# Kernel tuning notes

Measured on AMD Instinct MI355X. Metric: run time of the kernel, lower is better.

The kernel has to match this reference:

```python
import jax, jax.numpy as jnp
import numpy as np

N, E, G = 50000, 800000, 64
IN, HID, HEADS, OUT = 128, 64, 4, 128
NEG = 0.2  # PyG GATConv default negative_slope


def setup_inputs() -> dict:
    key = jax.random.key(0)
    ks = jax.random.split(key, 12)
    nrm = lambda k, shape, s: (jax.random.normal(k, shape, jnp.float32) * s)
    x = nrm(ks[0], (N, IN), 1.0)
    edge_index = jax.random.randint(ks[1], (2, E), 0, N)
    batch = jnp.sort(jax.random.randint(ks[2], (N,), 0, G))
    W1 = nrm(ks[3], (IN, HEADS * HID), IN ** -0.5)
    a1_src = nrm(ks[4], (HEADS, HID), HID ** -0.5)
    a1_dst = nrm(ks[5], (HEADS, HID), HID ** -0.5)
    b1 = jnp.zeros((HEADS * HID,), jnp.float32)
    W2 = nrm(ks[6], (HEADS * HID, OUT), (HEADS * HID) ** -0.5)
    a2_src = nrm(ks[7], (1, OUT), OUT ** -0.5)
    a2_dst = nrm(ks[8], (1, OUT), OUT ** -0.5)
    b2 = jnp.zeros((OUT,), jnp.float32)
    fc_W = nrm(ks[9], (OUT, OUT), OUT ** -0.5)
    fc_b = jnp.zeros((OUT,), jnp.float32)
    return dict(x=x, edge_index=edge_index, batch=batch, W1=W1, a1_src=a1_src,
                a1_dst=a1_dst, b1=b1, W2=W2, a2_src=a2_src, a2_dst=a2_dst,
                b2=b2, fc_W=fc_W, fc_b=fc_b)


def gat_conv(x, W, a_src, a_dst, b, src, dst, heads):
    n = x.shape[0]
    ch = W.shape[1] // heads
    h = (x @ W).reshape(n, heads, ch)                      # [n, H, C]
    al_s = jnp.einsum('nhc,hc->nh', h, a_src)              # per-node src logits
    al_d = jnp.einsum('nhc,hc->nh', h, a_dst)
    e = al_s[src] + al_d[dst]                              # [E, H]
    e = jnp.where(e > 0, e, NEG * e)                       # LeakyReLU
    # segment softmax over incoming edges of each dst node
    m = jax.lax.stop_gradient(jax.ops.segment_max(e, dst, num_segments=n))
    m = jnp.where(jnp.isfinite(m), m, 0.0)
    ex = jnp.exp(e - m[dst])
    s = jax.ops.segment_sum(ex, dst, num_segments=n)
    alpha = ex / (s[dst] + 1e-16)                          # [E, H]
    out = jax.ops.segment_sum(h[src] * alpha[..., None], dst, num_segments=n)
    return out.reshape(n, heads * ch) + b                  # concat heads + bias


def reference(x, edge_index, batch, W1, a1_src, a1_dst, b1, W2, a2_src, a2_dst, b2, fc_W, fc_b):
    loops = jnp.arange(N, dtype=edge_index.dtype)          # PyG adds self-loops
    src = jnp.concatenate([edge_index[0], loops])
    dst = jnp.concatenate([edge_index[1], loops])
    h = jax.nn.elu(gat_conv(x, W1, a1_src, a1_dst, b1, src, dst, HEADS))
    h = jax.nn.elu(gat_conv(h, W2, a2_src, a2_dst, b2, src, dst, 1))
    sums = jax.ops.segment_sum(h, batch, num_segments=G)
    cnt = jax.ops.segment_sum(jnp.ones((N,), h.dtype), batch, num_segments=G)
    pooled = sums / jnp.maximum(cnt, 1.0)[:, None]         # global mean pool
    return jax.nn.relu(pooled @ fc_W + fc_b)
```

## Files before the change

kernel.cpp:

```cpp
#include <hip/hip_runtime.h>
#include <math.h>

#define N_NODES 50000
#define N_EDGES 800000
#define N_GRAPHS 64
#define NEG 0.2f

typedef unsigned short us;
typedef us us2 __attribute__((ext_vector_type(2)));
typedef us us4 __attribute__((ext_vector_type(4)));
typedef us us8 __attribute__((ext_vector_type(8)));
typedef short bf16x8 __attribute__((ext_vector_type(8)));
typedef float f32x4 __attribute__((ext_vector_type(4)));

__device__ __forceinline__ us bf16rn(float f) {
  unsigned int u = __float_as_uint(f);
  u += 0x7FFFu + ((u >> 16) & 1u);
  return (us)(u >> 16);
}
__device__ __forceinline__ float bf2f(us h) {
  return __uint_as_float(((unsigned int)h) << 16);
}
__device__ __forceinline__ float readlane_f(float v, int l) {
  return __uint_as_float((unsigned)__builtin_amdgcn_readlane(__float_as_uint(v), l));
}

__global__ __launch_bounds__(256) void init_kernel(int* __restrict__ cnt,
                                                   float* __restrict__ psum) {
  int i = blockIdx.x * 256 + threadIdx.x;
  if (i < N_NODES) cnt[i] = 0;
  if (i < N_GRAPHS * 128) psum[i] = 0.f;
}

__global__ __launch_bounds__(256) void xsplit_kernel(const float* __restrict__ x,
                                                     us* __restrict__ xh,
                                                     us* __restrict__ xl,
                                                     int total4) {
  int i = blockIdx.x * 256 + threadIdx.x;
  if (i >= total4) return;
  float4 v = *(const float4*)&x[(size_t)i * 4];
  us h0 = bf16rn(v.x), h1 = bf16rn(v.y), h2 = bf16rn(v.z), h3 = bf16rn(v.w);
  us4 hv = {h0, h1, h2, h3};
  us4 lv = {bf16rn(v.x - bf2f(h0)), bf16rn(v.y - bf2f(h1)),
            bf16rn(v.z - bf2f(h2)), bf16rn(v.w - bf2f(h3))};
  *(us4*)&xh[(size_t)i * 4] = hv;
  *(us4*)&xl[(size_t)i * 4] = lv;
}

__global__ __launch_bounds__(256) void convW_kernel(
    const float* __restrict__ W1, const float* __restrict__ W2,
    us* __restrict__ w1h, us* __restrict__ w1l,
    us* __restrict__ w2h, us* __restrict__ w2l) {
  int idx = blockIdx.x * 256 + threadIdx.x;
  const float* W; us *oh, *ol; int K, N, li;
  if (idx < 128 * 256) {
    W = W1; oh = w1h; ol = w1l; K = 128; N = 256; li = idx;
  } else if (idx < 2 * 128 * 256) {
    W = W2; oh = w2h; ol = w2l; K = 256; N = 128; li = idx - 128 * 256;
  } else return;
  int n = li / K, k = li - n * K;
  float f = W[(size_t)k * N + n];
  us h = bf16rn(f);
  oh[li] = h;
  ol[li] = bf16rn(f - bf2f(h));
}

__global__ __launch_bounds__(256, 2) void gemm_bf16x3(
    const us* __restrict__ Agh, const us* __restrict__ Agl,
    const us* __restrict__ Bth, const us* __restrict__ Btl,
    us* __restrict__ C, int M, int N, int K) {
  __shared__ us smem[4][128][40];
  int t = threadIdx.x;
  int m0 = blockIdx.x * 128;
  int n0 = blockIdx.y * 128;
  int w = t >> 6, l = t & 63;
  int wr = w >> 1, wc = w & 1;
  int l15 = l & 15, g = l >> 4;

  f32x4 acc[4][4] = {};

  for (int kb = 0; kb < K; kb += 32) {
    us8 z = {};
    #pragma unroll
    for (int i = 0; i < 2; i++) {
      int slot = i * 256 + t;
      int row = slot >> 2, kq = slot & 3;
      size_t gi = (size_t)(m0 + row) * K + kb + kq * 8;
      bool ok = (m0 + row) < M;
      *(us8*)&smem[0][row][kq * 8] = ok ? *(const us8*)&Agh[gi] : z;
      *(us8*)&smem[1][row][kq * 8] = ok ? *(const us8*)&Agl[gi] : z;
    }
    #pragma unroll
    for (int i = 0; i < 2; i++) {
      int slot = i * 256 + t;
      int n = slot >> 2, kq = slot & 3;
      size_t gi = (size_t)(n0 + n) * K + kb + kq * 8;
      *(us8*)&smem[2][n][kq * 8] = *(const us8*)&Bth[gi];
      *(us8*)&smem[3][n][kq * 8] = *(const us8*)&Btl[gi];
    }
    __syncthreads();

    bf16x8 af[4], al4[4], bf[4], bl4[4];
    #pragma unroll
    for (int i = 0; i < 4; i++) {
      af[i]  = *(const bf16x8*)&smem[0][wr * 64 + i * 16 + l15][g * 8];
      al4[i] = *(const bf16x8*)&smem[1][wr * 64 + i * 16 + l15][g * 8];
      bf[i]  = *(const bf16x8*)&smem[2][wc * 64 + i * 16 + l15][g * 8];
      bl4[i] = *(const bf16x8*)&smem[3][wc * 64 + i * 16 + l15][g * 8];
    }
    #pragma unroll
    for (int i = 0; i < 4; i++)
      #pragma unroll
      for (int j = 0; j < 4; j++) {
        acc[i][j] = __builtin_amdgcn_mfma_f32_16x16x32_bf16(af[i], bf[j], acc[i][j], 0, 0, 0);
        acc[i][j] = __builtin_amdgcn_mfma_f32_16x16x32_bf16(af[i], bl4[j], acc[i][j], 0, 0, 0);
        acc[i][j] = __builtin_amdgcn_mfma_f32_16x16x32_bf16(al4[i], bf[j], acc[i][j], 0, 0, 0);
      }
    __syncthreads();
  }

  us* ct = &smem[0][0][0];
  #pragma unroll
  for (int i = 0; i < 4; i++)
    #pragma unroll
    for (int j = 0; j < 4; j++)
      #pragma unroll
      for (int r = 0; r < 4; r++) {
        int row = wr * 64 + i * 16 + g * 4 + r;
        int col = wc * 64 + j * 16 + l15;
        ct[row * 128 + col] = bf16rn(acc[i][j][r]);
      }
  __syncthreads();
  #pragma unroll
  for (int q = 0; q < 8; q++) {
    int slot = q * 256 + t;
    int row = slot >> 4, col8 = slot & 15;
    if (m0 + row < M) {
      us8 v = *(const us8*)&ct[row * 128 + col8 * 8];
      *(us8*)&C[(size_t)(m0 + row) * N + n0 + col8 * 8] = v;
    }
  }
}

__global__ __launch_bounds__(256) void logits1_kernel(
    const us* __restrict__ h1b, const float* __restrict__ a_src,
    const float* __restrict__ a_dst, float* __restrict__ al_s,
    float* __restrict__ al_d) {
  int idx = blockIdx.x * 256 + threadIdx.x;
  if (idx >= N_NODES * 4) return;
  int n = idx >> 2, h = idx & 3;
  const us* hp = &h1b[(size_t)n * 256 + h * 64];
  float ss = 0.f, sd = 0.f;
  #pragma unroll
  for (int i = 0; i < 8; i++) {
    us8 v = *(const us8*)&hp[i * 8];
    #pragma unroll
    for (int j = 0; j < 8; j++) {
      float f = bf2f(v[j]);
      ss += f * a_src[h * 64 + i * 8 + j];
      sd += f * a_dst[h * 64 + i * 8 + j];
    }
  }
  al_s[idx] = ss;
  al_d[idx] = sd;
}

__global__ __launch_bounds__(256) void logits2_kernel(
    const us* __restrict__ h2b, const float* __restrict__ a_src,
    const float* __restrict__ a_dst, float* __restrict__ al_s,
    float* __restrict__ al_d) {
  int n = blockIdx.x * 256 + threadIdx.x;
  if (n >= N_NODES) return;
  const us* hp = &h2b[(size_t)n * 128];
  float ss = 0.f, sd = 0.f;
  #pragma unroll
  for (int i = 0; i < 16; i++) {
    us8 v = *(const us8*)&hp[i * 8];
    #pragma unroll
    for (int j = 0; j < 8; j++) {
      float f = bf2f(v[j]);
      ss += f * a_src[i * 8 + j];
      sd += f * a_dst[i * 8 + j];
    }
  }
  al_s[n] = ss;
  al_d[n] = sd;
}

__global__ __launch_bounds__(256) void count_kernel(const int* __restrict__ dst,
                                                    int* __restrict__ cnt) {
  int e = blockIdx.x * 256 + threadIdx.x;
  if (e < N_EDGES) atomicAdd(&cnt[dst[e]], 1);
}

__global__ __launch_bounds__(256) void scan1_kernel(const int* __restrict__ cnt,
                                                    int* __restrict__ itmp,
                                                    int* __restrict__ bsum) {
  int i = blockIdx.x * 256 + threadIdx.x;
  int v = (i < N_NODES) ? cnt[i] : 0;
  int lane = threadIdx.x & 63, w = threadIdx.x >> 6;
  int s = v;
  #pragma unroll
  for (int off = 1; off < 64; off <<= 1) {
    int tv = __shfl_up(s, off);
    if (lane >= off) s += tv;
  }
  __shared__ int wsum[4];
  if (lane == 63) wsum[w] = s;
  __syncthreads();
  int add = 0;
  for (int p = 0; p < w; p++) add += wsum[p];
  s += add;
  if (i < N_NODES) itmp[i] = s;
  if (threadIdx.x == 255) bsum[blockIdx.x] = s;
}

__global__ __launch_bounds__(256) void scan2_kernel(const int* __restrict__ bsum,
                                                    int* __restrict__ boff,
                                                    int nb) {
  int t = threadIdx.x;
  int v = (t < nb) ? bsum[t] : 0;
  int lane = t & 63, w = t >> 6;
  int s = v;
  #pragma unroll
  for (int off = 1; off < 64; off <<= 1) {
    int tv = __shfl_up(s, off);
    if (lane >= off) s += tv;
  }
  __shared__ int wsum[4];
  if (lane == 63) wsum[w] = s;
  __syncthreads();
  int add = 0;
  for (int p = 0; p < w; p++) add += wsum[p];
  s += add;
  if (t < nb) boff[t] = s - v;
}

__global__ __launch_bounds__(256) void scan3_kernel(const int* __restrict__ cnt,
                                                    const int* __restrict__ itmp,
                                                    const int* __restrict__ boff,
                                                    int* __restrict__ rowst,
                                                    int* __restrict__ cursor) {
  int i = blockIdx.x * 256 + threadIdx.x;
  if (i < N_NODES) {
    int excl = itmp[i] - cnt[i] + boff[i >> 8];
    rowst[i] = excl;
    cursor[i] = excl;
  }
  if (i == 0) rowst[N_NODES] = N_EDGES;
}

__global__ __launch_bounds__(256) void scatter_kernel(
    const int* __restrict__ src, const int* __restrict__ dst,
    int* __restrict__ cursor, int* __restrict__ csr_src) {
  int e = blockIdx.x * 256 + threadIdx.x;
  if (e < N_EDGES) {
    int p = atomicAdd(&cursor[dst[e]], 1);
    csr_src[p] = src[e];
  }
}

__global__ __launch_bounds__(256) void agg1_kernel(
    const us* __restrict__ h1b, const float* __restrict__ al_s,
    const float* __restrict__ al_d, const int* __restrict__ rowst,
    const int* __restrict__ csrc, const float* __restrict__ b1,
    us* __restrict__ outh, us* __restrict__ outl) {
  int d = (blockIdx.x * 256 + threadIdx.x) >> 6;
  int lane = threadIdx.x & 63;
  if (d >= N_NODES) return;
  int head = lane >> 4;
  int c0 = lane * 4;
  int wsel = lane & 48;
  float ald = al_d[d * 4 + head];
  float wsum = 0.f, a0 = 0.f, a1 = 0.f, a2 = 0.f, a3 = 0.f;
  {
    float v = al_s[d * 4 + head] + ald;
    v = v > 0.f ? v : NEG * v;
    float w = __expf(v);
    us4 hv = *(const us4*)&h1b[(size_t)d * 256 + c0];
    wsum += w;
    a0 += w * bf2f(hv[0]); a1 += w * bf2f(hv[1]);
    a2 += w * bf2f(hv[2]); a3 += w * bf2f(hv[3]);
  }
  int beg = rowst[d], end = rowst[d + 1];
  int j = beg;
  for (; j + 16 <= end; j += 16) {
    int el = lane & 15;
    int sv = csrc[j + el];
    float v = al_s[sv * 4 + head] + ald;
    v = v > 0.f ? v : NEG * v;
    float wv = __expf(v);
    #pragma unroll
    for (int q = 0; q < 16; q += 4) {
      int s0 = __builtin_amdgcn_readlane(sv, q + 0);
      int s1 = __builtin_amdgcn_readlane(sv, q + 1);
      int s2 = __builtin_amdgcn_readlane(sv, q + 2);
      int s3 = __builtin_amdgcn_readlane(sv, q + 3);
      us4 h0 = *(const us4*)&h1b[(size_t)(unsigned)s0 * 256 + c0];
      us4 h1 = *(const us4*)&h1b[(size_t)(unsigned)s1 * 256 + c0];
      us4 h2 = *(const us4*)&h1b[(size_t)(unsigned)s2 * 256 + c0];
      us4 h3 = *(const us4*)&h1b[(size_t)(unsigned)s3 * 256 + c0];
      float w0 = __shfl(wv, q + 0 + wsel);
      float w1 = __shfl(wv, q + 1 + wsel);
      float w2 = __shfl(wv, q + 2 + wsel);
      float w3 = __shfl(wv, q + 3 + wsel);
      wsum += w0 + w1 + w2 + w3;
      a0 += w0 * bf2f(h0[0]) + w1 * bf2f(h1[0]) + w2 * bf2f(h2[0]) + w3 * bf2f(h3[0]);
      a1 += w0 * bf2f(h0[1]) + w1 * bf2f(h1[1]) + w2 * bf2f(h2[1]) + w3 * bf2f(h3[1]);
      a2 += w0 * bf2f(h0[2]) + w1 * bf2f(h1[2]) + w2 * bf2f(h2[2]) + w3 * bf2f(h3[2]);
      a3 += w0 * bf2f(h0[3]) + w1 * bf2f(h1[3]) + w2 * bf2f(h2[3]) + w3 * bf2f(h3[3]);
    }
  }
  int m = end - j;
  if (m > 0) {
    int el = lane & 15;
    int sv = csrc[j + (el < m ? el : 0)];
    float v = al_s[sv * 4 + head] + ald;
    v = v > 0.f ? v : NEG * v;
    float wv = __expf(v);
    for (int q = 0; q < m; q += 4) {
      int k0 = q, k1 = q + 1 < m ? q + 1 : 0, k2 = q + 2 < m ? q + 2 : 0,
          k3 = q + 3 < m ? q + 3 : 0;
      int s0 = __builtin_amdgcn_readlane(sv, k0);
      int s1 = __builtin_amdgcn_readlane(sv, k1);
      int s2 = __builtin_amdgcn_readlane(sv, k2);
      int s3 = __builtin_amdgcn_readlane(sv, k3);
      us4 h0 = *(const us4*)&h1b[(size_t)(unsigned)s0 * 256 + c0];
      us4 h1 = *(const us4*)&h1b[(size_t)(unsigned)s1 * 256 + c0];
      us4 h2 = *(const us4*)&h1b[(size_t)(unsigned)s2 * 256 + c0];
      us4 h3 = *(const us4*)&h1b[(size_t)(unsigned)s3 * 256 + c0];
      float w0 = __shfl(wv, k0 + wsel);
      float w1 = __shfl(wv, k1 + wsel);
      float w2 = __shfl(wv, k2 + wsel);
      float w3 = __shfl(wv, k3 + wsel);
      if (q + 1 >= m) w1 = 0.f;
      if (q + 2 >= m) w2 = 0.f;
      if (q + 3 >= m) w3 = 0.f;
      wsum += w0 + w1 + w2 + w3;
      a0 += w0 * bf2f(h0[0]) + w1 * bf2f(h1[0]) + w2 * bf2f(h2[0]) + w3 * bf2f(h3[0]);
      a1 += w0 * bf2f(h0[1]) + w1 * bf2f(h1[1]) + w2 * bf2f(h2[1]) + w3 * bf2f(h3[1]);
      a2 += w0 * bf2f(h0[2]) + w1 * bf2f(h1[2]) + w2 * bf2f(h2[2]) + w3 * bf2f(h3[2]);
      a3 += w0 * bf2f(h0[3]) + w1 * bf2f(h1[3]) + w2 * bf2f(h2[3]) + w3 * bf2f(h3[3]);
    }
  }
  float inv = 1.f / (wsum + 1e-16f);
  float4 bb = *(const float4*)&b1[c0];
  float o[4] = {a0 * inv + bb.x, a1 * inv + bb.y, a2 * inv + bb.z, a3 * inv + bb.w};
  us4 oh, ol;
  #pragma unroll
  for (int i = 0; i < 4; i++) {
    float e = o[i] > 0.f ? o[i] : expm1f(o[i]);
    us h = bf16rn(e);
    oh[i] = h;
    ol[i] = bf16rn(e - bf2f(h));
  }
  *(us4*)&outh[(size_t)d * 256 + c0] = oh;
  *(us4*)&outl[(size_t)d * 256 + c0] = ol;
}

__global__ __launch_bounds__(256) void agg2_kernel(
    const us* __restrict__ h2b, const float* __restrict__ al_s,
    const float* __restrict__ al_d, const int* __restrict__ rowst,
    const int* __restrict__ csrc, const float* __restrict__ b2,
    float* __restrict__ out) {
  int d = (blockIdx.x * 256 + threadIdx.x) >> 6;
  int lane = threadIdx.x & 63;
  if (d >= N_NODES) return;
  int c0 = lane * 2;
  float ald = al_d[d];
  float wsum = 0.f, a0 = 0.f, a1 = 0.f;
  {
    float v = al_s[d] + ald;
    v = v > 0.f ? v : NEG * v;
    float w = __expf(v);
    us2 hv = *(const us2*)&h2b[(size_t)d * 128 + c0];
    wsum += w;
    a0 += w * bf2f(hv[0]); a1 += w * bf2f(hv[1]);
  }
  int beg = rowst[d], end = rowst[d + 1];
  int j = beg;
  for (; j + 64 <= end; j += 64) {
    int sv = csrc[j + lane];
    float v = al_s[sv] + ald;
    v = v > 0.f ? v : NEG * v;
    float wv = __expf(v);
    for (int q = 0; q < 64; q += 4) {
      int s0 = __builtin_amdgcn_readlane(sv, q + 0);
      int s1 = __builtin_amdgcn_readlane(sv, q + 1);
      int s2 = __builtin_amdgcn_readlane(sv, q + 2);
      int s3 = __builtin_amdgcn_readlane(sv, q + 3);
      us2 h0 = *(const us2*)&h2b[(size_t)(unsigned)s0 * 128 + c0];
      us2 h1 = *(const us2*)&h2b[(size_t)(unsigned)s1 * 128 + c0];
      us2 h2 = *(const us2*)&h2b[(size_t)(unsigned)s2 * 128 + c0];
      us2 h3 = *(const us2*)&h2b[(size_t)(unsigned)s3 * 128 + c0];
      float w0 = readlane_f(wv, q + 0);
      float w1 = readlane_f(wv, q + 1);
      float w2 = readlane_f(wv, q + 2);
      float w3 = readlane_f(wv, q + 3);
      wsum += w0 + w1 + w2 + w3;
      a0 += w0 * bf2f(h0[0]) + w1 * bf2f(h1[0]) + w2 * bf2f(h2[0]) + w3 * bf2f(h3[0]);
      a1 += w0 * bf2f(h0[1]) + w1 * bf2f(h1[1]) + w2 * bf2f(h2[1]) + w3 * bf2f(h3[1]);
    }
  }
  int m = end - j;
  if (m > 0) {
    int sv = csrc[j + (lane < m ? lane : 0)];
    float v = al_s[sv] + ald;
    v = v > 0.f ? v : NEG * v;
    float wv = __expf(v);
    for (int q = 0; q < m; q += 4) {
      int k0 = q, k1 = q + 1 < m ? q + 1 : 0, k2 = q + 2 < m ? q + 2 : 0,
          k3 = q + 3 < m ? q + 3 : 0;
      int s0 = __builtin_amdgcn_readlane(sv, k0);
      int s1 = __builtin_amdgcn_readlane(sv, k1);
      int s2 = __builtin_amdgcn_readlane(sv, k2);
      int s3 = __builtin_amdgcn_readlane(sv, k3);
      us2 h0 = *(const us2*)&h2b[(size_t)(unsigned)s0 * 128 + c0];
      us2 h1 = *(const us2*)&h2b[(size_t)(unsigned)s1 * 128 + c0];
      us2 h2 = *(const us2*)&h2b[(size_t)(unsigned)s2 * 128 + c0];
      us2 h3 = *(const us2*)&h2b[(size_t)(unsigned)s3 * 128 + c0];
      float w0 = readlane_f(wv, k0);
      float w1 = readlane_f(wv, k1);
      float w2 = readlane_f(wv, k2);
      float w3 = readlane_f(wv, k3);
      if (q + 1 >= m) w1 = 0.f;
      if (q + 2 >= m) w2 = 0.f;
      if (q + 3 >= m) w3 = 0.f;
      wsum += w0 + w1 + w2 + w3;
      a0 += w0 * bf2f(h0[0]) + w1 * bf2f(h1[0]) + w2 * bf2f(h2[0]) + w3 * bf2f(h3[0]);
      a1 += w0 * bf2f(h0[1]) + w1 * bf2f(h1[1]) + w2 * bf2f(h2[1]) + w3 * bf2f(h3[1]);
    }
  }
  float inv = 1.f / (wsum + 1e-16f);
  float2 bb = *(const float2*)&b2[c0];
  float o0 = a0 * inv + bb.x, o1 = a1 * inv + bb.y;
  o0 = o0 > 0.f ? o0 : expm1f(o0);
  o1 = o1 > 0.f ? o1 : expm1f(o1);
  *(float2*)&out[(size_t)d * 128 + c0] = make_float2(o0, o1);
}

#define PNPB 128
__global__ __launch_bounds__(256) void pool_kernel(const float* __restrict__ y,
                                                   const int* __restrict__ batch,
                                                   float* __restrict__ psum) {
  int t = threadIdx.x;
  int lane32 = t & 31;
  int sub = t >> 5;
  int base = blockIdx.x * PNPB + sub * (PNPB / 8);
  int nend = base + PNPB / 8;
  if (nend > N_NODES) nend = N_NODES;
  float4 acc = make_float4(0.f, 0.f, 0.f, 0.f);
  int curg = -1;
  for (int n = base; n < nend; ++n) {
    int g = batch[n];
    if (g != curg) {
      if (curg >= 0) {
        float* p = &psum[curg * 128 + lane32 * 4];
        atomicAdd(p + 0, acc.x); atomicAdd(p + 1, acc.y);
        atomicAdd(p + 2, acc.z); atomicAdd(p + 3, acc.w);
      }
      acc = make_float4(0.f, 0.f, 0.f, 0.f);
      curg = g;
    }
    float4 v = *(const float4*)&y[(size_t)n * 128 + lane32 * 4];
    acc.x += v.x; acc.y += v.y; acc.z += v.z; acc.w += v.w;
  }
  if (curg >= 0) {
    float* p = &psum[curg * 128 + lane32 * 4];
    atomicAdd(p + 0, acc.x); atomicAdd(p + 1, acc.y);
    atomicAdd(p + 2, acc.z); atomicAdd(p + 3, acc.w);
  }
}

__global__ __launch_bounds__(128) void fc_kernel(
    const float* __restrict__ psum, const int* __restrict__ batch,
    const float* __restrict__ fcW, const float* __restrict__ fcb,
    float* __restrict__ out) {
  __shared__ float pr[128];
  __shared__ int bounds[2];
  int g = blockIdx.x, c = threadIdx.x;
  if (c < 2) {
    int target = g + c;
    int lo = 0, hi = N_NODES;
    while (lo < hi) {
      int mid = (lo + hi) >> 1;
      if (batch[mid] < target) lo = mid + 1; else hi = mid;
    }
    bounds[c] = lo;
  }
  __syncthreads();
  float cnt = (float)(bounds[1] - bounds[0]);
  cnt = cnt > 1.f ? cnt : 1.f;
  pr[c] = psum[g * 128 + c] / cnt;
  __syncthreads();
  float s = fcb[c];
  #pragma unroll 8
  for (int k = 0; k < 128; k++) s += pr[k] * fcW[k * 128 + c];
  out[g * 128 + c] = fmaxf(s, 0.f);
}

extern "C" void kernel_launch(void* const* d_in, const int* in_sizes, int n_in,
                              void* d_out, int out_size, void* d_ws,
                              size_t ws_size, hipStream_t stream) {
  const float* x      = (const float*)d_in[0];
  const int*   ei     = (const int*)d_in[1];
  const int*   batch  = (const int*)d_in[2];
  const float* W1     = (const float*)d_in[3];
  const float* a1_src = (const float*)d_in[4];
  const float* a1_dst = (const float*)d_in[5];
  const float* b1     = (const float*)d_in[6];
  const float* W2     = (const float*)d_in[7];
  const float* a2_src = (const float*)d_in[8];
  const float* a2_dst = (const float*)d_in[9];
  const float* b2     = (const float*)d_in[10];
  const float* fc_W   = (const float*)d_in[11];
  const float* fc_b   = (const float*)d_in[12];
  float* out = (float*)d_out;

  const int* srcp = ei;
  const int* dstp = ei + N_EDGES;
  const int NB = (N_NODES + 255) / 256;

  float* y    = (float*)d_ws;
  float* al1s = y + (size_t)N_NODES * 128;
  float* al1d = al1s + N_NODES * 4;
  float* al2s = al1d + N_NODES * 4;
  float* al2d = al2s + N_NODES;
  float* psum = al2d + N_NODES;
  us* xh   = (us*)(psum + N_GRAPHS * 128);
  us* xl   = xh + (size_t)N_NODES * 128;
  us* x2h  = xl + (size_t)N_NODES * 128;
  us* x2l  = x2h + (size_t)N_NODES * 256;
  us* h1b  = x2l + (size_t)N_NODES * 256;
  us* h2b  = h1b + (size_t)N_NODES * 256;
  us* w1th = h2b + (size_t)N_NODES * 128;
  us* w1tl = w1th + 256 * 128;
  us* w2th = w1tl + 256 * 128;
  us* w2tl = w2th + 128 * 256;
  int* cnt    = (int*)(w2tl + 128 * 256);
  int* bsum   = cnt + N_NODES;
  int* boff   = bsum + 256;
  int* itmp   = boff + 256;
  int* rowst  = itmp + N_NODES;
  int* cursor = rowst + N_NODES + 8;
  int* csrc   = cursor + N_NODES;
  size_t needed = (size_t)((char*)(csrc + N_EDGES) - (char*)d_ws);
  if (ws_size < needed) return;

  init_kernel<<<NB, 256, 0, stream>>>(cnt, psum);

  count_kernel<<<(N_EDGES + 255) / 256, 256, 0, stream>>>(dstp, cnt);
  scan1_kernel<<<NB, 256, 0, stream>>>(cnt, itmp, bsum);
  scan2_kernel<<<1, 256, 0, stream>>>(bsum, boff, NB);
  scan3_kernel<<<NB, 256, 0, stream>>>(cnt, itmp, boff, rowst, cursor);
  scatter_kernel<<<(N_EDGES + 255) / 256, 256, 0, stream>>>(srcp, dstp, cursor, csrc);

  xsplit_kernel<<<(N_NODES * 128 / 4 + 255) / 256, 256, 0, stream>>>(
      x, xh, xl, N_NODES * 128 / 4);
  convW_kernel<<<(2 * 128 * 256 + 255) / 256, 256, 0, stream>>>(
      W1, W2, w1th, w1tl, w2th, w2tl);

  gemm_bf16x3<<<dim3(391, 2), 256, 0, stream>>>(xh, xl, w1th, w1tl, h1b, N_NODES, 256, 128);
  logits1_kernel<<<(N_NODES * 4 + 255) / 256, 256, 0, stream>>>(h1b, a1_src, a1_dst, al1s, al1d);
  agg1_kernel<<<(N_NODES * 64 + 255) / 256, 256, 0, stream>>>(
      h1b, al1s, al1d, rowst, csrc, b1, x2h, x2l);

  gemm_bf16x3<<<dim3(391, 1), 256, 0, stream>>>(x2h, x2l, w2th, w2tl, h2b, N_NODES, 128, 256);
  logits2_kernel<<<(N_NODES + 255) / 256, 256, 0, stream>>>(h2b, a2_src, a2_dst, al2s, al2d);
  agg2_kernel<<<(N_NODES * 64 + 255) / 256, 256, 0, stream>>>(
      h2b, al2s, al2d, rowst, csrc, b2, y);

  pool_kernel<<<(N_NODES + PNPB - 1) / PNPB, 256, 0, stream>>>(y, batch, psum);
  fc_kernel<<<N_GRAPHS, 128, 0, stream>>>(psum, batch, fc_W, fc_b, out);
}
```

Baseline: 313.5 us.

## Fuse prep kernels, attention logits into GEMM epilogue, and merge scan passes

```diff
diff --git a/kernel.cpp b/kernel.cpp
--- a/kernel.cpp
+++ b/kernel.cpp
@@ -25,50 +25,45 @@
   return __uint_as_float((unsigned)__builtin_amdgcn_readlane(__float_as_uint(v), l));
 }
 
-__global__ __launch_bounds__(256) void init_kernel(int* __restrict__ cnt,
-                                                   float* __restrict__ psum) {
-  int i = blockIdx.x * 256 + threadIdx.x;
-  if (i < N_NODES) cnt[i] = 0;
-  if (i < N_GRAPHS * 128) psum[i] = 0.f;
-}
-
-__global__ __launch_bounds__(256) void xsplit_kernel(const float* __restrict__ x,
-                                                     us* __restrict__ xh,
-                                                     us* __restrict__ xl,
-                                                     int total4) {
-  int i = blockIdx.x * 256 + threadIdx.x;
-  if (i >= total4) return;
-  float4 v = *(const float4*)&x[(size_t)i * 4];
-  us h0 = bf16rn(v.x), h1 = bf16rn(v.y), h2 = bf16rn(v.z), h3 = bf16rn(v.w);
-  us4 hv = {h0, h1, h2, h3};
-  us4 lv = {bf16rn(v.x - bf2f(h0)), bf16rn(v.y - bf2f(h1)),
-            bf16rn(v.z - bf2f(h2)), bf16rn(v.w - bf2f(h3))};
-  *(us4*)&xh[(size_t)i * 4] = hv;
-  *(us4*)&xl[(size_t)i * 4] = lv;
-}
-
-__global__ __launch_bounds__(256) void convW_kernel(
+__global__ __launch_bounds__(256) void prep_kernel(
+    const float* __restrict__ x, us* __restrict__ xh, us* __restrict__ xl,
     const float* __restrict__ W1, const float* __restrict__ W2,
     us* __restrict__ w1h, us* __restrict__ w1l,
-    us* __restrict__ w2h, us* __restrict__ w2l) {
-  int idx = blockIdx.x * 256 + threadIdx.x;
-  const float* W; us *oh, *ol; int K, N, li;
-  if (idx < 128 * 256) {
-    W = W1; oh = w1h; ol = w1l; K = 128; N = 256; li = idx;
-  } else if (idx < 2 * 128 * 256) {
-    W = W2; oh = w2h; ol = w2l; K = 256; N = 128; li = idx - 128 * 256;
-  } else return;
-  int n = li / K, k = li - n * K;
-  float f = W[(size_t)k * N + n];
-  us h = bf16rn(f);
-  oh[li] = h;
-  ol[li] = bf16rn(f - bf2f(h));
+    us* __restrict__ w2h, us* __restrict__ w2l,
+    int* __restrict__ cnt, float* __restrict__ psum) {
+  int bid = blockIdx.x, t = threadIdx.x;
+  if (bid < 6250) {
+    int i = bid * 256 + t;
+    float4 v = *(const float4*)&x[(size_t)i * 4];
+    us h0 = bf16rn(v.x), h1 = bf16rn(v.y), h2 = bf16rn(v.z), h3 = bf16rn(v.w);
+    us4 hv = {h0, h1, h2, h3};
+    us4 lv = {bf16rn(v.x - bf2f(h0)), bf16rn(v.y - bf2f(h1)),
+              bf16rn(v.z - bf2f(h2)), bf16rn(v.w - bf2f(h3))};
+    *(us4*)&xh[(size_t)i * 4] = hv;
+    *(us4*)&xl[(size_t)i * 4] = lv;
+  } else if (bid < 6506) {
+    int idx = (bid - 6250) * 256 + t;
+    const float* W; us *oh, *ol; int K, N, li;
+    if (idx < 128 * 256) { W = W1; oh = w1h; ol = w1l; K = 128; N = 256; li = idx; }
+    else { W = W2; oh = w2h; ol = w2l; K = 256; N = 128; li = idx - 128 * 256; }
+    int n = li / K, k = li - n * K;
+    float f = W[(size_t)k * N + n];
+    us h = bf16rn(f);
+    oh[li] = h;
+    ol[li] = bf16rn(f - bf2f(h));
+  } else {
+    int i = (bid - 6506) * 256 + t;
+    if (i < N_NODES) cnt[i] = 0;
+    if (i < N_GRAPHS * 128) psum[i] = 0.f;
+  }
 }
 
 __global__ __launch_bounds__(256, 2) void gemm_bf16x3(
     const us* __restrict__ Agh, const us* __restrict__ Agl,
     const us* __restrict__ Bth, const us* __restrict__ Btl,
-    us* __restrict__ C, int M, int N, int K) {
+    us* __restrict__ C, int M, int N, int K, int heads,
+    const float* __restrict__ a_src, const float* __restrict__ a_dst,
+    float* __restrict__ al_s, float* __restrict__ al_d) {
   __shared__ us smem[4][128][40];
   int t = threadIdx.x;
   int m0 = blockIdx.x * 128;
@@ -140,51 +135,48 @@
       *(us8*)&C[(size_t)(m0 + row) * N + n0 + col8 * 8] = v;
     }
   }
-}
-
-__global__ __launch_bounds__(256) void logits1_kernel(
-    const us* __restrict__ h1b, const float* __restrict__ a_src,
-    const float* __restrict__ a_dst, float* __restrict__ al_s,
-    float* __restrict__ al_d) {
-  int idx = blockIdx.x * 256 + threadIdx.x;
-  if (idx >= N_NODES * 4) return;
-  int n = idx >> 2, h = idx & 3;
-  const us* hp = &h1b[(size_t)n * 256 + h * 64];
-  float ss = 0.f, sd = 0.f;
-  #pragma unroll
-  for (int i = 0; i < 8; i++) {
-    us8 v = *(const us8*)&hp[i * 8];
-    #pragma unroll
-    for (int j = 0; j < 8; j++) {
-      float f = bf2f(v[j]);
-      ss += f * a_src[h * 64 + i * 8 + j];
-      sd += f * a_dst[h * 64 + i * 8 + j];
-    }
-  }
-  al_s[idx] = ss;
-  al_d[idx] = sd;
-}
-
-__global__ __launch_bounds__(256) void logits2_kernel(
-    const us* __restrict__ h2b, const float* __restrict__ a_src,
-    const float* __restrict__ a_dst, float* __restrict__ al_s,
-    float* __restrict__ al_d) {
-  int n = blockIdx.x * 256 + threadIdx.x;
-  if (n >= N_NODES) return;
-  const us* hp = &h2b[(size_t)n * 128];
-  float ss = 0.f, sd = 0.f;
-  #pragma unroll
-  for (int i = 0; i < 16; i++) {
-    us8 v = *(const us8*)&hp[i * 8];
-    #pragma unroll
-    for (int j = 0; j < 8; j++) {
-      float f = bf2f(v[j]);
-      ss += f * a_src[i * 8 + j];
-      sd += f * a_dst[i * 8 + j];
-    }
-  }
-  al_s[n] = ss;
-  al_d[n] = sd;
+
+  if (heads == 4) {
+    int r = t & 127, hs = t >> 7;
+    int row = m0 + r;
+    if (row < M) {
+      int head = blockIdx.y * 2 + hs;
+      const float* as = &a_src[head * 64];
+      const float* ad = &a_dst[head * 64];
+      float ss = 0.f, sd = 0.f;
+      #pragma unroll
+      for (int k8 = 0; k8 < 8; k8++) {
+        us8 v = *(const us8*)&ct[r * 128 + hs * 64 + k8 * 8];
+        #pragma unroll
+        for (int j = 0; j < 8; j++) {
+          float f = bf2f(v[j]);
+          ss += f * as[k8 * 8 + j];
+          sd += f * ad[k8 * 8 + j];
+        }
+      }
+      al_s[row * 4 + head] = ss;
+      al_d[row * 4 + head] = sd;
+    }
+  } else if (heads == 1) {
+    if (t < 128) {
+      int row = m0 + t;
+      if (row < M) {
+        float ss = 0.f, sd = 0.f;
+        #pragma unroll
+        for (int k8 = 0; k8 < 16; k8++) {
+          us8 v = *(const us8*)&ct[t * 128 + k8 * 8];
+          #pragma unroll
+          for (int j = 0; j < 8; j++) {
+            float f = bf2f(v[j]);
+            ss += f * a_src[k8 * 8 + j];
+            sd += f * a_dst[k8 * 8 + j];
+          }
+        }
+        al_s[row] = ss;
+        al_d[row] = sd;
+      }
+    }
+  }
 }
 
 __global__ __launch_bounds__(256) void count_kernel(const int* __restrict__ dst,
@@ -215,35 +207,25 @@
   if (threadIdx.x == 255) bsum[blockIdx.x] = s;
 }
 
-__global__ __launch_bounds__(256) void scan2_kernel(const int* __restrict__ bsum,
-                                                    int* __restrict__ boff,
+__global__ __launch_bounds__(256) void scan3_kernel(const int* __restrict__ cnt,
+                                                    const int* __restrict__ itmp,
+                                                    const int* __restrict__ bsum,
+                                                    int* __restrict__ rowst,
+                                                    int* __restrict__ cursor,
                                                     int nb) {
   int t = threadIdx.x;
-  int v = (t < nb) ? bsum[t] : 0;
   int lane = t & 63, w = t >> 6;
+  int v = (t < nb && t < blockIdx.x) ? bsum[t] : 0;
   int s = v;
   #pragma unroll
-  for (int off = 1; off < 64; off <<= 1) {
-    int tv = __shfl_up(s, off);
-    if (lane >= off) s += tv;
-  }
-  __shared__ int wsum[4];
-  if (lane == 63) wsum[w] = s;
+  for (int off = 1; off < 64; off <<= 1) s += __shfl_xor(s, off);
+  __shared__ int partial[4];
+  if (lane == 0) partial[w] = s;
   __syncthreads();
-  int add = 0;
-  for (int p = 0; p < w; p++) add += wsum[p];
-  s += add;
-  if (t < nb) boff[t] = s - v;
-}
-
-__global__ __launch_bounds__(256) void scan3_kernel(const int* __restrict__ cnt,
-                                                    const int* __restrict__ itmp,
-                                                    const int* __restrict__ boff,
-                                                    int* __restrict__ rowst,
-                                                    int* __restrict__ cursor) {
-  int i = blockIdx.x * 256 + threadIdx.x;
+  int boff = partial[0] + partial[1] + partial[2] + partial[3];
+  int i = blockIdx.x * 256 + t;
   if (i < N_NODES) {
-    int excl = itmp[i] - cnt[i] + boff[i >> 8];
+    int excl = itmp[i] - cnt[i] + boff;
     rowst[i] = excl;
     cursor[i] = excl;
   }
@@ -547,26 +529,23 @@
   size_t needed = (size_t)((char*)(csrc + N_EDGES) - (char*)d_ws);
   if (ws_size < needed) return;
 
-  init_kernel<<<NB, 256, 0, stream>>>(cnt, psum);
+  prep_kernel<<<6702, 256, 0, stream>>>(x, xh, xl, W1, W2, w1th, w1tl, w2th,
+                                        w2tl, cnt, psum);
 
   count_kernel<<<(N_EDGES + 255) / 256, 256, 0, stream>>>(dstp, cnt);
   scan1_kernel<<<NB, 256, 0, stream>>>(cnt, itmp, bsum);
-  scan2_kernel<<<1, 256, 0, stream>>>(bsum, boff, NB);
-  scan3_kernel<<<NB, 256, 0, stream>>>(cnt, itmp, boff, rowst, cursor);
+  scan3_kernel<<<NB, 256, 0, stream>>>(cnt, itmp, bsum, rowst, cursor, NB);
   scatter_kernel<<<(N_EDGES + 255) / 256, 256, 0, stream>>>(srcp, dstp, cursor, csrc);
 
-  xsplit_kernel<<<(N_NODES * 128 / 4 + 255) / 256, 256, 0, stream>>>(
-      x, xh, xl, N_NODES * 128 / 4);
-  convW_kernel<<<(2 * 128 * 256 + 255) / 256, 256, 0, stream>>>(
-      W1, W2, w1th, w1tl, w2th, w2tl);
-
-  gemm_bf16x3<<<dim3(391, 2), 256, 0, stream>>>(xh, xl, w1th, w1tl, h1b, N_NODES, 256, 128);
-  logits1_kernel<<<(N_NODES * 4 + 255) / 256, 256, 0, stream>>>(h1b, a1_src, a1_dst, al1s, al1d);
+  gemm_bf16x3<<<dim3(391, 2), 256, 0, stream>>>(xh, xl, w1th, w1tl, h1b,
+                                                N_NODES, 256, 128, 4, a1_src,
+                                                a1_dst, al1s, al1d);
   agg1_kernel<<<(N_NODES * 64 + 255) / 256, 256, 0, stream>>>(
       h1b, al1s, al1d, rowst, csrc, b1, x2h, x2l);
 
-  gemm_bf16x3<<<dim3(391, 1), 256, 0, stream>>>(x2h, x2l, w2th, w2tl, h2b, N_NODES, 128, 256);
-  logits2_kernel<<<(N_NODES + 255) / 256, 256, 0, stream>>>(h2b, a2_src, a2_dst, al2s, al2d);
+  gemm_bf16x3<<<dim3(391, 1), 256, 0, stream>>>(x2h, x2l, w2th, w2tl, h2b,
+                                                N_NODES, 128, 256, 1, a2_src,
+                                                a2_dst, al2s, al2d);
   agg2_kernel<<<(N_NODES * 64 + 255) / 256, 256, 0, stream>>>(
       h2b, al2s, al2d, rowst, csrc, b2, y);
 
```

After: 281.9 us. 10.1% less time.
